# Performance work log

Hardware: AMD Instinct MI355X
Metric: run time of the kernel (lower is better)

## Reference

```python
import jax, jax.numpy as jnp
import numpy as np

FP8_MAX = 448.0  # max representable magnitude in float8_e4m3fn
EPS = 1e-12


def setup_inputs() -> dict:
    key = jax.random.key(0)
    k1, k2, k3 = jax.random.split(key, 3)
    B, S, DIN, DOUT = 8, 4096, 1024, 1024
    x = jax.random.normal(k1, (B, S, DIN), dtype=jnp.float32)
    weight = jax.random.normal(k2, (DOUT, DIN), dtype=jnp.float32) * (1.0 / np.sqrt(DIN))
    bias = jax.random.normal(k3, (DOUT,), dtype=jnp.float32) * 0.01
    return {"x": x, "weight": weight, "bias": bias}


def _quantize_fp8(t):
    # per-tensor dynamic scale: amax / 448, clamped
    scale = jnp.maximum(jnp.max(jnp.abs(t)) / FP8_MAX, EPS).astype(jnp.float32)
    t_fp8 = (t / scale).astype(jnp.float8_e4m3fn)
    return t_fp8, scale


def reference(x, weight, bias):
    in_features = weight.shape[1]
    out_features = weight.shape[0]
    # quantize weights (mirrors quantize_weights())
    w_fp8, w_scale = _quantize_fp8(weight)
    # dynamic activation quantization
    x_flat = x.reshape(-1, in_features)  # [M, K]
    x_fp8, x_scale = _quantize_fp8(x_flat)
    # scaled fp8 GEMM: accumulate in fp32, apply per-tensor scales (torch._scaled_mm)
    out = jnp.einsum(
        "mk,nk->mn",
        x_fp8.astype(jnp.float32),
        w_fp8.astype(jnp.float32),
    ) * (x_scale * w_scale)
    out = out.reshape(*x.shape[:-1], out_features)
    return out + bias
```

## Files before the change

kernel.cpp:

```cpp
#include <hip/hip_runtime.h>
#include <cstdint>
#include <cstddef>

typedef float f32x4 __attribute__((ext_vector_type(4)));
typedef long  lx2   __attribute__((ext_vector_type(2)));

#define PXB 1024
#define PWB 64
#define QXB 2048
#define QWB 128

__device__ __forceinline__ void async_copy16(const uint8_t* g, uint8_t* s) {
    __builtin_amdgcn_global_load_lds(
        (const __attribute__((address_space(1))) void*)g,
        (__attribute__((address_space(3))) void*)s,
        16 , 0 , 0 );
}

__device__ __forceinline__ float block_max(float m, float* scr) {
#pragma unroll
    for (int o = 32; o > 0; o >>= 1) m = fmaxf(m, __shfl_down(m, o, 64));
    const int lane = threadIdx.x & 63, wid = threadIdx.x >> 6;
    if (lane == 0) scr[wid] = m;
    __syncthreads();
    const int nw = blockDim.x >> 6;
    m = scr[0];
    for (int j = 1; j < nw; ++j) m = fmaxf(m, scr[j]);
    return m;
}

__global__ void amax_partials(const float4* __restrict__ x, int nx4,
                              const float4* __restrict__ w, int nw4,
                              float* __restrict__ part) {
    __shared__ float scr[8];
    const int b = blockIdx.x;
    const float4* p;
    int n4, nb, bi;
    if (b < PXB) { p = x; n4 = nx4; nb = PXB; bi = b; }
    else         { p = w; n4 = nw4; nb = PWB; bi = b - PXB; }
    float m = 0.0f;
    for (int i = bi * blockDim.x + threadIdx.x; i < n4; i += nb * blockDim.x) {
        float4 v = p[i];
        m = fmaxf(m, fmaxf(fmaxf(fabsf(v.x), fabsf(v.y)),
                           fmaxf(fabsf(v.z), fabsf(v.w))));
    }
    m = block_max(m, scr);
    if (threadIdx.x == 0) part[b] = m;
}

__global__ void quant_fused(const float4* __restrict__ x, int nx16,
                            const float4* __restrict__ w, int nw16,
                            const float* __restrict__ part,
                            int4* __restrict__ xq, int4* __restrict__ wq) {
    __shared__ float scr[8];
    const int b = blockIdx.x;
    const float4* in;
    const float* pp;
    int4* out;
    int n16, nb, bi, np;
    if (b < QXB) { in = x; n16 = nx16; nb = QXB; bi = b;       pp = part;       np = PXB; out = xq; }
    else         { in = w; n16 = nw16; nb = QWB; bi = b - QXB; pp = part + PXB; np = PWB; out = wq; }

    float m = 0.0f;
    for (int i = threadIdx.x; i < np; i += blockDim.x) m = fmaxf(m, pp[i]);
    m = block_max(m, scr);
    const float r = 1.0f / fmaxf(m / 448.0f, 1e-12f);

    for (int i = bi * blockDim.x + threadIdx.x; i < n16; i += nb * blockDim.x) {
        int4 o;
#pragma unroll
        for (int j = 0; j < 4; ++j) {
            float4 v = in[i * 4 + j];
            int p = 0;
            p = __builtin_amdgcn_cvt_pk_fp8_f32(v.x * r, v.y * r, p, false);
            p = __builtin_amdgcn_cvt_pk_fp8_f32(v.z * r, v.w * r, p, true);
            ((int*)&o)[j] = p;
        }
        out[i] = o;
    }
}

__global__ __launch_bounds__(256) void gemm_fp8_kernel(
    const uint8_t* __restrict__ A,
    const uint8_t* __restrict__ B,
    const float* __restrict__ bias,
    const float* __restrict__ part,
    float* __restrict__ out,
    int M, int N, int K) {
    __shared__ long lds64[2048];
    uint8_t* Abase = (uint8_t*)lds64;
    uint8_t* Bbase = Abase + 8192;

    const int tid  = threadIdx.x;
    const int l    = tid & 63;
    const int w    = tid >> 6;
    const int lm   = l & 15;
    const int quad = l >> 4;
    const int wm   = (w >> 1) * 64;
    const int wn   = (w & 1) * 64;

    const size_t am0 = (size_t)blockIdx.y * 128;
    const size_t bn0 = (size_t)blockIdx.x * 128;

    float* scr = (float*)lds64;
    float mx = 0.0f, mw = 0.0f;
    for (int i = tid; i < PXB; i += 256) mx = fmaxf(mx, part[i]);
    for (int i = tid; i < PWB; i += 256) mw = fmaxf(mw, part[PXB + i]);
    mx = block_max(mx, scr);
    mw = block_max(mw, scr + 8);
    const float scale = fmaxf(mx / 448.0f, 1e-12f) * fmaxf(mw / 448.0f, 1e-12f);
    __syncthreads();

    f32x4 acc[4][4];
#pragma unroll
    for (int i = 0; i < 4; ++i)
#pragma unroll
        for (int j = 0; j < 4; ++j) acc[i][j] = (f32x4)0.0f;

    const int slot0 = w * 64 + l;

    for (int kt = 0; kt < K; kt += 64) {
#pragma unroll
        for (int i = 0; i < 2; ++i) {
            const int s    = i * 256 + slot0;
            const int row  = s >> 2;
            const int chnk = s & 3;
            async_copy16(A + (am0 + row) * K + kt + chnk * 16,
                         Abase + (i * 4 + w) * 1024);
            async_copy16(B + (bn0 + row) * K + kt + chnk * 16,
                         Bbase + (i * 4 + w) * 1024);
        }
        __syncthreads();

        lx2 a[4], b[4];
#pragma unroll
        for (int t = 0; t < 4; ++t) {
            a[t] = *(const lx2*)&lds64[(wm + t * 16 + lm) * 8 + quad * 2];
            b[t] = *(const lx2*)&lds64[1024 + (wn + t * 16 + lm) * 8 + quad * 2];
        }
#pragma unroll
        for (int ks = 0; ks < 2; ++ks)
#pragma unroll
            for (int mt = 0; mt < 4; ++mt)
#pragma unroll
                for (int nt = 0; nt < 4; ++nt)
                    acc[mt][nt] = __builtin_amdgcn_mfma_f32_16x16x32_fp8_fp8(
                        a[mt][ks], b[nt][ks], acc[mt][nt], 0, 0, 0);
        __syncthreads();
    }

#pragma unroll
    for (int nt = 0; nt < 4; ++nt) {
        const int n = (int)bn0 + wn + nt * 16 + lm;
        const float bv = bias[n];
#pragma unroll
        for (int mt = 0; mt < 4; ++mt) {
            const size_t mrow = am0 + wm + mt * 16 + quad * 4;
#pragma unroll
            for (int r = 0; r < 4; ++r) {
                out[(mrow + r) * (size_t)N + n] = acc[mt][nt][r] * scale + bv;
            }
        }
    }
}

extern "C" void kernel_launch(void* const* d_in, const int* in_sizes, int n_in,
                              void* d_out, int out_size, void* d_ws,
                              size_t ws_size, hipStream_t stream) {
    const float* x      = (const float*)d_in[0];
    const float* weight = (const float*)d_in[1];
    const float* bias   = (const float*)d_in[2];
    float* out          = (float*)d_out;

    const int nx = in_sizes[0];
    const int nw = in_sizes[1];
    const int N  = in_sizes[2];
    const int K  = nw / N;
    const int M  = nx / K;

    float* part     = (float*)d_ws;
    uint8_t* x_fp8  = (uint8_t*)d_ws + 8192;
    uint8_t* w_fp8  = x_fp8 + (size_t)nx;

    amax_partials<<<PXB + PWB, 256, 0, stream>>>(
        (const float4*)x, nx / 4, (const float4*)weight, nw / 4, part);
    quant_fused<<<QXB + QWB, 256, 0, stream>>>(
        (const float4*)x, nx / 16, (const float4*)weight, nw / 16, part,
        (int4*)x_fp8, (int4*)w_fp8);
    gemm_fp8_kernel<<<dim3(N / 128, M / 128), 256, 0, stream>>>(
        x_fp8, w_fp8, bias, part, out, M, N, K);
}
```

Baseline: 319.6 us.

## Fuse activation FP8 quantization into GEMM A-tile load with register prefetch

Drops the separate pass that quantizes x to FP8. The GEMM now reads fp32 activations, converts them to FP8 in registers and writes them into LDS, prefetching the next K-tile into registers while the MFMAs run. The weight quantization pass is split into its own small kernel, and block indices are remapped for better L2 locality. This removes one full read of x and one fp8 write/read round trip, but it quadruples A-tile global traffic inside the GEMM because each row is re-read as fp32 by every N-block (8 of them), and it uses more registers.

```diff
diff --git a/kernel.cpp b/kernel.cpp
--- a/kernel.cpp
+++ b/kernel.cpp
@@ -7,8 +7,7 @@
 
 #define PXB 1024
 #define PWB 64
-#define QXB 2048
-#define QWB 128
+#define QWB 64
 
 __device__ __forceinline__ void async_copy16(const uint8_t* g, uint8_t* s) {
     __builtin_amdgcn_global_load_lds(
@@ -48,40 +47,33 @@
     if (threadIdx.x == 0) part[b] = m;
 }
 
-__global__ void quant_fused(const float4* __restrict__ x, int nx16,
-                            const float4* __restrict__ w, int nw16,
-                            const float* __restrict__ part,
-                            int4* __restrict__ xq, int4* __restrict__ wq) {
+__global__ void quant_w_kernel(const float4* __restrict__ w, int nw16,
+                               const float* __restrict__ part,
+                               int4* __restrict__ wq) {
     __shared__ float scr[8];
-    const int b = blockIdx.x;
-    const float4* in;
-    const float* pp;
-    int4* out;
-    int n16, nb, bi, np;
-    if (b < QXB) { in = x; n16 = nx16; nb = QXB; bi = b;       pp = part;       np = PXB; out = xq; }
-    else         { in = w; n16 = nw16; nb = QWB; bi = b - QXB; pp = part + PXB; np = PWB; out = wq; }
-
     float m = 0.0f;
-    for (int i = threadIdx.x; i < np; i += blockDim.x) m = fmaxf(m, pp[i]);
+    for (int i = threadIdx.x; i < PWB; i += blockDim.x)
+        m = fmaxf(m, part[PXB + i]);
     m = block_max(m, scr);
     const float r = 1.0f / fmaxf(m / 448.0f, 1e-12f);
 
-    for (int i = bi * blockDim.x + threadIdx.x; i < n16; i += nb * blockDim.x) {
+    for (int i = blockIdx.x * blockDim.x + threadIdx.x; i < nw16;
+         i += QWB * blockDim.x) {
         int4 o;
 #pragma unroll
         for (int j = 0; j < 4; ++j) {
-            float4 v = in[i * 4 + j];
+            float4 v = w[i * 4 + j];
             int p = 0;
             p = __builtin_amdgcn_cvt_pk_fp8_f32(v.x * r, v.y * r, p, false);
             p = __builtin_amdgcn_cvt_pk_fp8_f32(v.z * r, v.w * r, p, true);
             ((int*)&o)[j] = p;
         }
-        out[i] = o;
+        wq[i] = o;
     }
 }
 
 __global__ __launch_bounds__(256) void gemm_fp8_kernel(
-    const uint8_t* __restrict__ A,
+    const float* __restrict__ A32,
     const uint8_t* __restrict__ B,
     const float* __restrict__ bias,
     const float* __restrict__ part,
@@ -99,8 +91,25 @@
     const int wm   = (w >> 1) * 64;
     const int wn   = (w & 1) * 64;
 
-    const size_t am0 = (size_t)blockIdx.y * 128;
-    const size_t bn0 = (size_t)blockIdx.x * 128;
+    int bx = blockIdx.x, by = blockIdx.y;
+    if (gridDim.x == 8) {
+        const int lin = blockIdx.x + (blockIdx.y << 3);
+        const int c = lin & 7;
+        const int k = lin >> 3;
+        bx = k & 7;
+        by = (k & ~7) | c;
+    }
+    const size_t am0 = (size_t)by * 128;
+    const size_t bn0 = (size_t)bx * 128;
+
+    const int arow = tid >> 4;
+    const int acol = (tid & 15) * 4;
+    const float* aptr = A32 + (am0 + arow) * (size_t)K + acol;
+
+    f32x4 av[8];
+#pragma unroll
+    for (int j = 0; j < 8; ++j)
+        av[j] = *(const f32x4*)(aptr + (size_t)j * 16 * K);
 
     float* scr = (float*)lds64;
     float mx = 0.0f, mw = 0.0f;
@@ -108,7 +117,10 @@
     for (int i = tid; i < PWB; i += 256) mw = fmaxf(mw, part[PXB + i]);
     mx = block_max(mx, scr);
     mw = block_max(mw, scr + 8);
-    const float scale = fmaxf(mx / 448.0f, 1e-12f) * fmaxf(mw / 448.0f, 1e-12f);
+    const float sx = fmaxf(mx / 448.0f, 1e-12f);
+    const float sw = fmaxf(mw / 448.0f, 1e-12f);
+    const float scale = sx * sw;
+    const float rq = 1.0f / sx;
     __syncthreads();
 
     f32x4 acc[4][4];
@@ -125,10 +137,15 @@
             const int s    = i * 256 + slot0;
             const int row  = s >> 2;
             const int chnk = s & 3;
-            async_copy16(A + (am0 + row) * K + kt + chnk * 16,
-                         Abase + (i * 4 + w) * 1024);
             async_copy16(B + (bn0 + row) * K + kt + chnk * 16,
                          Bbase + (i * 4 + w) * 1024);
+        }
+#pragma unroll
+        for (int j = 0; j < 8; ++j) {
+            int p = 0;
+            p = __builtin_amdgcn_cvt_pk_fp8_f32(av[j].x * rq, av[j].y * rq, p, false);
+            p = __builtin_amdgcn_cvt_pk_fp8_f32(av[j].z * rq, av[j].w * rq, p, true);
+            *(int*)(Abase + (j * 16 + arow) * 64 + acol) = p;
         }
         __syncthreads();
 
@@ -137,6 +154,12 @@
         for (int t = 0; t < 4; ++t) {
             a[t] = *(const lx2*)&lds64[(wm + t * 16 + lm) * 8 + quad * 2];
             b[t] = *(const lx2*)&lds64[1024 + (wn + t * 16 + lm) * 8 + quad * 2];
+        }
+        if (kt + 64 < K) {
+            const float* ap = aptr + (kt + 64);
+#pragma unroll
+            for (int j = 0; j < 8; ++j)
+                av[j] = *(const f32x4*)(ap + (size_t)j * 16 * K);
         }
 #pragma unroll
         for (int ks = 0; ks < 2; ++ks)
@@ -179,14 +202,12 @@
     const int M  = nx / K;
 
     float* part     = (float*)d_ws;
-    uint8_t* x_fp8  = (uint8_t*)d_ws + 8192;
-    uint8_t* w_fp8  = x_fp8 + (size_t)nx;
+    uint8_t* w_fp8  = (uint8_t*)d_ws + 8192;
 
     amax_partials<<<PXB + PWB, 256, 0, stream>>>(
         (const float4*)x, nx / 4, (const float4*)weight, nw / 4, part);
-    quant_fused<<<QXB + QWB, 256, 0, stream>>>(
-        (const float4*)x, nx / 16, (const float4*)weight, nw / 16, part,
-        (int4*)x_fp8, (int4*)w_fp8);
+    quant_w_kernel<<<QWB, 256, 0, stream>>>(
+        (const float4*)weight, nw / 16, part, (int4*)w_fp8);
     gemm_fp8_kernel<<<dim3(N / 128, M / 128), 256, 0, stream>>>(
-        x_fp8, w_fp8, bias, part, out, M, N, K);
-}
+        x, w_fp8, bias, part, out, M, N, K);
+}
```

New measurement: 297.3 us. 7.0% less time.
